# Kernel tuning notes

Hardware: AMD Instinct MI355X
Metric: run time of the kernel (lower is better)

The kernel has to match this reference:

```python
import jax, jax.numpy as jnp
import numpy as np

N = 4194304  # nodes
B = 16384    # graphs
D = 2        # spatial dim
EPS = 1e-12  # F.normalize eps


def _mlp(x, W1, b1, W2, b2, W3, b3, W4, b4, W5, b5):
    h = jax.nn.relu(x @ W1.T + b1)
    h = jax.nn.relu(h @ W2.T + b2)
    h = jax.nn.relu(h @ W3.T + b3)
    h = jax.nn.relu(h @ W4.T + b4)
    return h @ W5.T + b5  # [N,1]


def setup_inputs() -> dict:
    key = jax.random.key(0)
    ks = jax.random.split(key, 16)
    inp = {
        "t": jax.random.normal(ks[0], (N,), jnp.float32),
        "pos": jax.random.normal(ks[1], (N, D), jnp.float32),
        "poi_t": jax.random.normal(ks[2], (B,), jnp.float32),
        "poi_pos": jax.random.normal(ks[3], (B, D), jnp.float32),
        "batch": jnp.sort(jax.random.randint(ks[4], (N,), 0, B, jnp.int64)),
    }
    dims = [(10, 3), (20, 10), (10, 20), (5, 10), (1, 5)]
    for i, (o, ii) in enumerate(dims):
        s = 1.0 / np.sqrt(ii)
        inp[f"W{i+1}"] = jax.random.uniform(ks[5 + 2 * i], (o, ii), jnp.float32, -s, s)
        inp[f"b{i+1}"] = jax.random.uniform(ks[6 + 2 * i], (o,), jnp.float32, -s, s)
    return inp


def reference(t, pos, poi_t, poi_pos, batch, W1, b1, W2, b2, W3, b3, W4, b4, W5, b5):
    num_seg = poi_t.shape[0]
    diff_t = t - poi_t[batch]                      # [N]
    diff_pos = pos - poi_pos[batch]                # [N,D]
    r2 = jnp.sum(diff_pos ** 2, axis=1)            # [N]
    centroid = jax.ops.segment_sum(pos, batch, num_segments=num_seg)  # [B,D]
    diff_centroid = (centroid - poi_pos)[batch]    # [N,D]
    cosine = jnp.sum(diff_pos * diff_centroid, axis=1) / jnp.sqrt(
        r2 * jnp.sum(diff_centroid ** 2, axis=1))  # [N]
    feats = jnp.stack((diff_t, r2, cosine), axis=1)  # [N,3]
    weights = _mlp(feats, W1, b1, W2, b2, W3, b3, W4, b4, W5, b5)  # [N,1]
    norm = jnp.maximum(jnp.linalg.norm(diff_pos, axis=1, keepdims=True), EPS)
    unit = diff_pos / norm                         # F.normalize(diff_pos, dim=1)
    return jax.ops.segment_sum(weights * unit, batch, num_segments=num_seg)  # [B,D]
```

## Files before the change

kernel.cpp:

```cpp
#include <hip/hip_runtime.h>

#define NN 4194304
#define NB 16384

typedef _Float16 half4 __attribute__((ext_vector_type(4)));
typedef float floatx4 __attribute__((ext_vector_type(4)));
typedef unsigned int uint;

__device__ __forceinline__ uint pk_u32(float lo, float hi) {
  return __builtin_bit_cast(uint, __builtin_amdgcn_cvt_pkrtz(lo, hi));
}

__device__ __forceinline__ half4 relu_cvt(floatx4 d) {
  uint2 u;
  u.x = pk_u32(d[0], d[1]);
  u.y = pk_u32(d[2], d[3]);
  half4 h = __builtin_bit_cast(half4, u);
  return __builtin_elementwise_max(h, half4{0, 0, 0, 0});
}

template <int CTRL>
__device__ __forceinline__ float dpp_add(float x) {
  int y = __builtin_amdgcn_update_dpp(0, __builtin_bit_cast(int, x), CTRL,
                                      0xf, 0xf, true);
  return x + __builtin_bit_cast(float, y);
}
__device__ __forceinline__ float wave_sum(float x) {
  x = dpp_add<0x111>(x);
  x = dpp_add<0x112>(x);
  x = dpp_add<0x114>(x);
  x = dpp_add<0x118>(x);
  x = dpp_add<0x142>(x);
  x = dpp_add<0x143>(x);
  return x;
}

__device__ __forceinline__ void seg_atomic_add2(int b, float vx, float vy,
                                                float* __restrict__ out) {
  const int lane = threadIdx.x & 63;
  int b0 = __builtin_amdgcn_readfirstlane(b);
  if (__ballot(b == b0) == ~0ull) {
    float sx = wave_sum(vx);
    float sy = wave_sum(vy);
    if (lane == 63) {
      atomicAdd(&out[2 * b0], sx);
      atomicAdd(&out[2 * b0 + 1], sy);
    }
    return;
  }
  int bprev = __shfl_up(b, 1);
  bool head = (lane == 0) || (b != bprev);
  unsigned long long hb = __ballot(head);
  unsigned long long mask_le = hb << (63 - lane);
  int run_start = lane - __clzll(mask_le);
  float sx = vx, sy = vy;
#pragma unroll
  for (int off = 1; off < 64; off <<= 1) {
    float ox = __shfl_up(sx, off);
    float oy = __shfl_up(sy, off);
    if (lane - off >= run_start) { sx += ox; sy += oy; }
  }
  int bnext = __shfl_down(b, 1);
  bool tail = (lane == 63) || (b != bnext);
  if (tail) {
    atomicAdd(&out[2 * b], sx);
    atomicAdd(&out[2 * b + 1], sy);
  }
}

__global__ __launch_bounds__(256) void centroid_kernel(
    const float2* __restrict__ pos, const int* __restrict__ batch,
    float* __restrict__ csum) {
  int base = blockIdx.x * 1024 + threadIdx.x;
  int bi[4];
  float2 pv[4];
#pragma unroll
  for (int r = 0; r < 4; ++r) {
    bi[r] = batch[base + r * 256];
    pv[r] = pos[base + r * 256];
  }
#pragma unroll
  for (int r = 0; r < 4; ++r) seg_atomic_add2(bi[r], pv[r].x, pv[r].y, csum);
}

__global__ void prepack_kernel(
    const float* __restrict__ W1, const float* __restrict__ W2,
    const float* __restrict__ W3, const float* __restrict__ W4,
    const float* __restrict__ W5, const float* __restrict__ B1,
    const float* __restrict__ B2, const float* __restrict__ B3,
    const float* __restrict__ B4, const float* __restrict__ B5,
    uint2* __restrict__ Wf, float* __restrict__ csum,
    float* __restrict__ out) {
  if (blockIdx.x >= 3) {
    int z = (blockIdx.x - 3) * 256 + threadIdx.x;
    float4 zero{0.f, 0.f, 0.f, 0.f};
    if (z < 8192) ((float4*)csum)[z] = zero;
    else ((float4*)out)[z - 8192] = zero;
    return;
  }
  int p = blockIdx.x * 256 + threadIdx.x;
  if (p >= 448) return;
  int tile = p >> 6, lane = p & 63, row = lane & 15, kb = (lane >> 4) * 4;
  float v[4];
#pragma unroll
  for (int i = 0; i < 4; ++i) {
    int k = kb + i;
    float x = 0.f;
    switch (tile) {
      case 0:
        if (row < 10 && k < 3) x = W1[row * 3 + k];
        if (k == 3) { if (row < 10) x = B1[row]; else if (row == 10) x = 1.f; }
        break;
      case 1:
        if (k < 10) x = W2[row * 10 + k];
        else if (k == 10) x = B2[row];
        break;
      case 2:
        if (row < 4 && k < 10) x = W2[(16 + row) * 10 + k];
        if (k == 10) { if (row < 4) x = B2[16 + row]; else if (row == 4) x = 1.f; }
        break;
      case 3:
        if (row < 10 && k < 16) x = W3[row * 20 + k];
        break;
      case 4:
        if (row < 10 && k < 4) x = W3[row * 20 + 16 + k];
        if (k == 4) { if (row < 10) x = B3[row]; else if (row == 10) x = 1.f; }
        break;
      case 5:
        if (row < 5 && k < 10) x = W4[row * 10 + k];
        if (k == 10) { if (row < 5) x = B4[row]; else if (row == 5) x = 1.f; }
        break;
      default:
        if (row == 0 && k < 5) x = W5[k];
        if (row == 0 && k == 5) x = B5[0];
        break;
    }
    v[i] = x;
  }
  Wf[p] = uint2{pk_u32(v[0], v[1]), pk_u32(v[2], v[3])};
}

__device__ __forceinline__ floatx4 mfma16(half4 a, half4 b, floatx4 c) {
  return __builtin_amdgcn_mfma_f32_16x16x16f16(a, b, c, 0, 0, 0);
}

__global__ __launch_bounds__(256, 3) void main_kernel(
    const float* __restrict__ t, const float2* __restrict__ pos,
    const float* __restrict__ poi_t, const float2* __restrict__ poi_pos,
    const int* __restrict__ batch, const float2* __restrict__ csum2,
    const uint2* __restrict__ Wf, float* __restrict__ out) {
  const int tid = threadIdx.x;
  const int lane = tid & 63;
  const int col = lane & 15;
  const int koct = lane >> 4;

  int base = blockIdx.x * 1024 + tid;
  int bi[4];
  float tvv[4];
  float2 pv[4];
#pragma unroll
  for (int r = 0; r < 4; ++r) {
    bi[r] = batch[base + r * 256];
    tvv[r] = t[base + r * 256];
    pv[r] = pos[base + r * 256];
  }
  float2 ppr[4], csr[4];
  float ptg[4];
#pragma unroll
  for (int r = 0; r < 4; ++r) {
    ppr[r] = poi_pos[bi[r]];
    csr[r] = csum2[bi[r]];
    ptg[r] = poi_t[bi[r]];
  }

  half4 wa[7];
#pragma unroll
  for (int k = 0; k < 7; ++k)
    wa[k] = __builtin_bit_cast(half4, Wf[k * 64 + lane]);
  floatx4 cz{0.f, 0.f, 0.f, 0.f};

#pragma unroll
  for (int rp = 0; rp < 2; ++rp) {
    float dpx[2], dpy[2], f1v[2], invr[2];
    int fx[2], fy[2];
#pragma unroll
    for (int u = 0; u < 2; ++u) {
      int r = rp * 2 + u;
      float f0 = tvv[r] - ptg[r];
      float dcx = csr[r].x - ppr[r].x;
      float dcy = csr[r].y - ppr[r].y;
      float invc = rsqrtf(dcx * dcx + dcy * dcy);
      dpx[u] = pv[r].x - ppr[r].x;
      dpy[u] = pv[r].y - ppr[r].y;
      f1v[u] = dpx[u] * dpx[u] + dpy[u] * dpy[u];
      invr[u] = rsqrtf(f1v[u]);
      float f2 = (dpx[u] * dcx + dpy[u] * dcy) * invc * invr[u];
      fx[u] = (int)pk_u32(f0, f1v[u]);
      fy[u] = (int)pk_u32(f2, 1.0f);
    }

    half4 b1[8];
#pragma unroll
    for (int u = 0; u < 2; ++u)
#pragma unroll
      for (int g = 0; g < 4; ++g) {
        int src = g * 16 + col;
        uint2 fr;
        fr.x = (uint)__shfl(fx[u], src);
        fr.y = (uint)__shfl(fy[u], src);
        b1[u * 4 + g] = __builtin_bit_cast(half4, fr);
      }

    floatx4 d[8];
    half4 a[8];
#pragma unroll
    for (int c = 0; c < 8; ++c) d[c] = mfma16(wa[0], b1[c], cz);
#pragma unroll
    for (int c = 0; c < 8; ++c) a[c] = relu_cvt(d[c]);

    floatx4 d2[8];
    half4 a3a[8], a3b[8];
#pragma unroll
    for (int c = 0; c < 8; ++c) d2[c] = mfma16(wa[1], a[c], cz);
#pragma unroll
    for (int c = 0; c < 8; ++c) a3a[c] = relu_cvt(d2[c]);
#pragma unroll
    for (int c = 0; c < 8; ++c) d2[c] = mfma16(wa[2], a[c], cz);
#pragma unroll
    for (int c = 0; c < 8; ++c) a3b[c] = relu_cvt(d2[c]);

#pragma unroll
    for (int c = 0; c < 8; ++c) d[c] = mfma16(wa[3], a3a[c], cz);
#pragma unroll
    for (int c = 0; c < 8; ++c) d[c] = mfma16(wa[4], a3b[c], d[c]);
#pragma unroll
    for (int c = 0; c < 8; ++c) a[c] = relu_cvt(d[c]);

#pragma unroll
    for (int c = 0; c < 8; ++c) d[c] = mfma16(wa[5], a[c], cz);
#pragma unroll
    for (int c = 0; c < 8; ++c) a[c] = relu_cvt(d[c]);

#pragma unroll
    for (int c = 0; c < 8; ++c) d[c] = mfma16(wa[6], a[c], cz);

#pragma unroll
    for (int u = 0; u < 2; ++u) {
      float wg0 = __shfl(d[u * 4 + 0][0], col);
      float wg1 = __shfl(d[u * 4 + 1][0], col);
      float wg2 = __shfl(d[u * 4 + 2][0], col);
      float wg3 = __shfl(d[u * 4 + 3][0], col);
      float w = wg0;
      w = (koct == 1) ? wg1 : w;
      w = (koct == 2) ? wg2 : w;
      w = (koct == 3) ? wg3 : w;
      float invn = (f1v[u] > 0.f) ? invr[u] : 0.f;
      seg_atomic_add2(bi[rp * 2 + u], w * dpx[u] * invn, w * dpy[u] * invn,
                      out);
    }
  }
}

extern "C" void kernel_launch(void* const* d_in, const int* in_sizes, int n_in,
                              void* d_out, int out_size, void* d_ws,
                              size_t ws_size, hipStream_t stream) {
  const float* t = (const float*)d_in[0];
  const float2* pos = (const float2*)d_in[1];
  const float* poi_t = (const float*)d_in[2];
  const float2* poi_pos = (const float2*)d_in[3];
  const int* batch = (const int*)d_in[4];
  const float* W1 = (const float*)d_in[5];
  const float* B1 = (const float*)d_in[6];
  const float* W2 = (const float*)d_in[7];
  const float* B2 = (const float*)d_in[8];
  const float* W3 = (const float*)d_in[9];
  const float* B3 = (const float*)d_in[10];
  const float* W4 = (const float*)d_in[11];
  const float* B4 = (const float*)d_in[12];
  const float* W5 = (const float*)d_in[13];
  const float* B5 = (const float*)d_in[14];
  float* out = (float*)d_out;

  float* csum = (float*)d_ws;
  uint2* Wf = (uint2*)(csum + 2 * NB);

  prepack_kernel<<<67, 256, 0, stream>>>(W1, W2, W3, W4, W5, B1, B2, B3, B4,
                                         B5, Wf, csum, out);
  centroid_kernel<<<NN / 1024, 256, 0, stream>>>(pos, batch, csum);
  main_kernel<<<NN / 1024, 256, 0, stream>>>(t, pos, poi_t, poi_pos, batch,
                                             (const float2*)csum, Wf, out);
}
```

Before: 50.23 us.

## Use persistent grid with software-prefetched next tile in centroid and main kernels

Both the centroid and main kernels now launch a fixed grid of 768 blocks that loop over 4096 work units instead of one block per unit. Each iteration prefetches the next unit's batch, t and pos values, and the main kernel also prefetches the gathered poi and centroid values, before the current unit's MLP and atomics. The goal is to hide global-load latency behind compute and cut block-launch overhead. The cost is higher register pressure from the double-buffered state, which could lower occupancy under the launch bounds of 3.

```diff
diff --git a/kernel.cpp b/kernel.cpp
--- a/kernel.cpp
+++ b/kernel.cpp
@@ -2,6 +2,8 @@
 
 #define NN 4194304
 #define NB 16384
+#define GRIDP 768
+#define NUNITS 4096
 
 typedef _Float16 half4 __attribute__((ext_vector_type(4)));
 typedef float floatx4 __attribute__((ext_vector_type(4)));
@@ -71,16 +73,36 @@
 __global__ __launch_bounds__(256) void centroid_kernel(
     const float2* __restrict__ pos, const int* __restrict__ batch,
     float* __restrict__ csum) {
-  int base = blockIdx.x * 1024 + threadIdx.x;
-  int bi[4];
-  float2 pv[4];
+  const int tid = threadIdx.x;
+  int u = blockIdx.x;
+  int biA[4];
+  float2 pvA[4];
+  int base = u * 1024 + tid;
 #pragma unroll
   for (int r = 0; r < 4; ++r) {
-    bi[r] = batch[base + r * 256];
-    pv[r] = pos[base + r * 256];
-  }
-#pragma unroll
-  for (int r = 0; r < 4; ++r) seg_atomic_add2(bi[r], pv[r].x, pv[r].y, csum);
+    biA[r] = batch[base + r * 256];
+    pvA[r] = pos[base + r * 256];
+  }
+  for (; u < NUNITS; u += GRIDP) {
+    int un = u + GRIDP;
+    int biB[4];
+    float2 pvB[4];
+    if (un < NUNITS) {
+      int nb = un * 1024 + tid;
+#pragma unroll
+      for (int r = 0; r < 4; ++r) {
+        biB[r] = batch[nb + r * 256];
+        pvB[r] = pos[nb + r * 256];
+      }
+    }
+#pragma unroll
+    for (int r = 0; r < 4; ++r)
+      seg_atomic_add2(biA[r], pvA[r].x, pvA[r].y, csum);
+    if (un < NUNITS) {
+#pragma unroll
+      for (int r = 0; r < 4; ++r) { biA[r] = biB[r]; pvA[r] = pvB[r]; }
+    }
+  }
 }
 
 __global__ void prepack_kernel(
@@ -154,109 +176,158 @@
   const int col = lane & 15;
   const int koct = lane >> 4;
 
-  int base = blockIdx.x * 1024 + tid;
-  int bi[4];
-  float tvv[4];
-  float2 pv[4];
-#pragma unroll
-  for (int r = 0; r < 4; ++r) {
-    bi[r] = batch[base + r * 256];
-    tvv[r] = t[base + r * 256];
-    pv[r] = pos[base + r * 256];
-  }
-  float2 ppr[4], csr[4];
-  float ptg[4];
-#pragma unroll
-  for (int r = 0; r < 4; ++r) {
-    ppr[r] = poi_pos[bi[r]];
-    csr[r] = csum2[bi[r]];
-    ptg[r] = poi_t[bi[r]];
-  }
-
   half4 wa[7];
 #pragma unroll
   for (int k = 0; k < 7; ++k)
     wa[k] = __builtin_bit_cast(half4, Wf[k * 64 + lane]);
   floatx4 cz{0.f, 0.f, 0.f, 0.f};
 
-#pragma unroll
-  for (int rp = 0; rp < 2; ++rp) {
-    float dpx[2], dpy[2], f1v[2], invr[2];
-    int fx[2], fy[2];
-#pragma unroll
-    for (int u = 0; u < 2; ++u) {
-      int r = rp * 2 + u;
-      float f0 = tvv[r] - ptg[r];
-      float dcx = csr[r].x - ppr[r].x;
-      float dcy = csr[r].y - ppr[r].y;
+  int u = blockIdx.x;
+  int biA[4];
+  float tvA[4];
+  float2 pvA[4];
+  {
+    int base = u * 1024 + tid;
+#pragma unroll
+    for (int r = 0; r < 4; ++r) {
+      biA[r] = batch[base + r * 256];
+      tvA[r] = t[base + r * 256];
+      pvA[r] = pos[base + r * 256];
+    }
+  }
+  float2 ppA[4], csA[4];
+  float ptA[4];
+#pragma unroll
+  for (int r = 0; r < 4; ++r) {
+    ppA[r] = poi_pos[biA[r]];
+    csA[r] = csum2[biA[r]];
+    ptA[r] = poi_t[biA[r]];
+  }
+
+  for (; u < NUNITS; u += GRIDP) {
+    const int un = u + GRIDP;
+    const bool hn = (un < NUNITS);
+
+    int biB[4];
+    float tvB[4];
+    float2 pvB[4];
+    if (hn) {
+      int nb = un * 1024 + tid;
+#pragma unroll
+      for (int r = 0; r < 4; ++r) {
+        biB[r] = batch[nb + r * 256];
+        tvB[r] = t[nb + r * 256];
+        pvB[r] = pos[nb + r * 256];
+      }
+    }
+
+    float dpx[4], dpy[4], f1v[4], invr[4];
+    int fx[4], fy[4];
+#pragma unroll
+    for (int r = 0; r < 4; ++r) {
+      float f0 = tvA[r] - ptA[r];
+      float dcx = csA[r].x - ppA[r].x;
+      float dcy = csA[r].y - ppA[r].y;
       float invc = rsqrtf(dcx * dcx + dcy * dcy);
-      dpx[u] = pv[r].x - ppr[r].x;
-      dpy[u] = pv[r].y - ppr[r].y;
-      f1v[u] = dpx[u] * dpx[u] + dpy[u] * dpy[u];
-      invr[u] = rsqrtf(f1v[u]);
-      float f2 = (dpx[u] * dcx + dpy[u] * dcy) * invc * invr[u];
-      fx[u] = (int)pk_u32(f0, f1v[u]);
-      fy[u] = (int)pk_u32(f2, 1.0f);
-    }
-
-    half4 b1[8];
-#pragma unroll
-    for (int u = 0; u < 2; ++u)
-#pragma unroll
-      for (int g = 0; g < 4; ++g) {
-        int src = g * 16 + col;
-        uint2 fr;
-        fr.x = (uint)__shfl(fx[u], src);
-        fr.y = (uint)__shfl(fy[u], src);
-        b1[u * 4 + g] = __builtin_bit_cast(half4, fr);
-      }
-
-    floatx4 d[8];
-    half4 a[8];
-#pragma unroll
-    for (int c = 0; c < 8; ++c) d[c] = mfma16(wa[0], b1[c], cz);
-#pragma unroll
-    for (int c = 0; c < 8; ++c) a[c] = relu_cvt(d[c]);
-
-    floatx4 d2[8];
-    half4 a3a[8], a3b[8];
-#pragma unroll
-    for (int c = 0; c < 8; ++c) d2[c] = mfma16(wa[1], a[c], cz);
-#pragma unroll
-    for (int c = 0; c < 8; ++c) a3a[c] = relu_cvt(d2[c]);
-#pragma unroll
-    for (int c = 0; c < 8; ++c) d2[c] = mfma16(wa[2], a[c], cz);
-#pragma unroll
-    for (int c = 0; c < 8; ++c) a3b[c] = relu_cvt(d2[c]);
-
-#pragma unroll
-    for (int c = 0; c < 8; ++c) d[c] = mfma16(wa[3], a3a[c], cz);
-#pragma unroll
-    for (int c = 0; c < 8; ++c) d[c] = mfma16(wa[4], a3b[c], d[c]);
-#pragma unroll
-    for (int c = 0; c < 8; ++c) a[c] = relu_cvt(d[c]);
-
-#pragma unroll
-    for (int c = 0; c < 8; ++c) d[c] = mfma16(wa[5], a[c], cz);
-#pragma unroll
-    for (int c = 0; c < 8; ++c) a[c] = relu_cvt(d[c]);
-
-#pragma unroll
-    for (int c = 0; c < 8; ++c) d[c] = mfma16(wa[6], a[c], cz);
-
-#pragma unroll
-    for (int u = 0; u < 2; ++u) {
-      float wg0 = __shfl(d[u * 4 + 0][0], col);
-      float wg1 = __shfl(d[u * 4 + 1][0], col);
-      float wg2 = __shfl(d[u * 4 + 2][0], col);
-      float wg3 = __shfl(d[u * 4 + 3][0], col);
-      float w = wg0;
-      w = (koct == 1) ? wg1 : w;
-      w = (koct == 2) ? wg2 : w;
-      w = (koct == 3) ? wg3 : w;
-      float invn = (f1v[u] > 0.f) ? invr[u] : 0.f;
-      seg_atomic_add2(bi[rp * 2 + u], w * dpx[u] * invn, w * dpy[u] * invn,
+      dpx[r] = pvA[r].x - ppA[r].x;
+      dpy[r] = pvA[r].y - ppA[r].y;
+      f1v[r] = dpx[r] * dpx[r] + dpy[r] * dpy[r];
+      invr[r] = rsqrtf(f1v[r]);
+      float f2 = (dpx[r] * dcx + dpy[r] * dcy) * invc * invr[r];
+      fx[r] = (int)pk_u32(f0, f1v[r]);
+      fy[r] = (int)pk_u32(f2, 1.0f);
+    }
+
+    float wv[4];
+#pragma unroll
+    for (int rp = 0; rp < 2; ++rp) {
+      half4 b1[8];
+#pragma unroll
+      for (int uu = 0; uu < 2; ++uu)
+#pragma unroll
+        for (int g = 0; g < 4; ++g) {
+          int src = g * 16 + col;
+          uint2 fr;
+          fr.x = (uint)__shfl(fx[rp * 2 + uu], src);
+          fr.y = (uint)__shfl(fy[rp * 2 + uu], src);
+          b1[uu * 4 + g] = __builtin_bit_cast(half4, fr);
+        }
+
+      floatx4 d[8];
+      half4 a[8];
+#pragma unroll
+      for (int c = 0; c < 8; ++c) d[c] = mfma16(wa[0], b1[c], cz);
+#pragma unroll
+      for (int c = 0; c < 8; ++c) a[c] = relu_cvt(d[c]);
+
+      floatx4 d2[8];
+      half4 a3a[8], a3b[8];
+#pragma unroll
+      for (int c = 0; c < 8; ++c) d2[c] = mfma16(wa[1], a[c], cz);
+#pragma unroll
+      for (int c = 0; c < 8; ++c) a3a[c] = relu_cvt(d2[c]);
+#pragma unroll
+      for (int c = 0; c < 8; ++c) d2[c] = mfma16(wa[2], a[c], cz);
+#pragma unroll
+      for (int c = 0; c < 8; ++c) a3b[c] = relu_cvt(d2[c]);
+
+#pragma unroll
+      for (int c = 0; c < 8; ++c) d[c] = mfma16(wa[3], a3a[c], cz);
+#pragma unroll
+      for (int c = 0; c < 8; ++c) d[c] = mfma16(wa[4], a3b[c], d[c]);
+#pragma unroll
+      for (int c = 0; c < 8; ++c) a[c] = relu_cvt(d[c]);
+
+#pragma unroll
+      for (int c = 0; c < 8; ++c) d[c] = mfma16(wa[5], a[c], cz);
+#pragma unroll
+      for (int c = 0; c < 8; ++c) a[c] = relu_cvt(d[c]);
+
+#pragma unroll
+      for (int c = 0; c < 8; ++c) d[c] = mfma16(wa[6], a[c], cz);
+
+#pragma unroll
+      for (int uu = 0; uu < 2; ++uu) {
+        float wg0 = __shfl(d[uu * 4 + 0][0], col);
+        float wg1 = __shfl(d[uu * 4 + 1][0], col);
+        float wg2 = __shfl(d[uu * 4 + 2][0], col);
+        float wg3 = __shfl(d[uu * 4 + 3][0], col);
+        float w = wg0;
+        w = (koct == 1) ? wg1 : w;
+        w = (koct == 2) ? wg2 : w;
+        w = (koct == 3) ? wg3 : w;
+        wv[rp * 2 + uu] = w;
+      }
+    }
+
+    float2 ppB[4], csB[4];
+    float ptB[4];
+    if (hn) {
+#pragma unroll
+      for (int r = 0; r < 4; ++r) {
+        ppB[r] = poi_pos[biB[r]];
+        csB[r] = csum2[biB[r]];
+        ptB[r] = poi_t[biB[r]];
+      }
+    }
+
+#pragma unroll
+    for (int r = 0; r < 4; ++r) {
+      float invn = (f1v[r] > 0.f) ? invr[r] : 0.f;
+      seg_atomic_add2(biA[r], wv[r] * dpx[r] * invn, wv[r] * dpy[r] * invn,
                       out);
+    }
+
+    if (hn) {
+#pragma unroll
+      for (int r = 0; r < 4; ++r) {
+        biA[r] = biB[r];
+        tvA[r] = tvB[r];
+        pvA[r] = pvB[r];
+        ppA[r] = ppB[r];
+        csA[r] = csB[r];
+        ptA[r] = ptB[r];
+      }
     }
   }
 }
@@ -286,7 +357,7 @@
 
   prepack_kernel<<<67, 256, 0, stream>>>(W1, W2, W3, W4, W5, B1, B2, B3, B4,
                                          B5, Wf, csum, out);
-  centroid_kernel<<<NN / 1024, 256, 0, stream>>>(pos, batch, csum);
-  main_kernel<<<NN / 1024, 256, 0, stream>>>(t, pos, poi_t, poi_pos, batch,
-                                             (const float2*)csum, Wf, out);
-}
+  centroid_kernel<<<GRIDP, 256, 0, stream>>>(pos, batch, csum);
+  main_kernel<<<GRIDP, 256, 0, stream>>>(t, pos, poi_t, poi_pos, batch,
+                                         (const float2*)csum, Wf, out);
+}
```

Measured after the change: 61.90 us. 1.23x slower.

## Fuse centroid and main kernels using a persistent grid barrier

Applied to the files above, without the earlier changes.

Merges the centroid segment-sum kernel and the MLP kernel into one persistent kernel of 1024 blocks, each handling 4096 nodes. Blocks first atomically accumulate centroids, then synchronise through a global atomic counter barrier before running the MLP. Batch and pos values stay in registers, so they are not re-read and one launch is saved. The barrier relies on all 1024 blocks being co-resident (256 CUs at 4 blocks each), and the larger per-thread register arrays add register pressure.

```diff
diff --git a/kernel.cpp b/kernel.cpp
--- a/kernel.cpp
+++ b/kernel.cpp
@@ -2,6 +2,7 @@
 
 #define NN 4194304
 #define NB 16384
+#define GRIDP 1024
 
 typedef _Float16 half4 __attribute__((ext_vector_type(4)));
 typedef float floatx4 __attribute__((ext_vector_type(4)));
@@ -68,21 +69,6 @@
   }
 }
 
-__global__ __launch_bounds__(256) void centroid_kernel(
-    const float2* __restrict__ pos, const int* __restrict__ batch,
-    float* __restrict__ csum) {
-  int base = blockIdx.x * 1024 + threadIdx.x;
-  int bi[4];
-  float2 pv[4];
-#pragma unroll
-  for (int r = 0; r < 4; ++r) {
-    bi[r] = batch[base + r * 256];
-    pv[r] = pos[base + r * 256];
-  }
-#pragma unroll
-  for (int r = 0; r < 4; ++r) seg_atomic_add2(bi[r], pv[r].x, pv[r].y, csum);
-}
-
 __global__ void prepack_kernel(
     const float* __restrict__ W1, const float* __restrict__ W2,
     const float* __restrict__ W3, const float* __restrict__ W4,
@@ -90,7 +76,7 @@
     const float* __restrict__ B2, const float* __restrict__ B3,
     const float* __restrict__ B4, const float* __restrict__ B5,
     uint2* __restrict__ Wf, float* __restrict__ csum,
-    float* __restrict__ out) {
+    float* __restrict__ out, uint* __restrict__ bar) {
   if (blockIdx.x >= 3) {
     int z = (blockIdx.x - 3) * 256 + threadIdx.x;
     float4 zero{0.f, 0.f, 0.f, 0.f};
@@ -99,7 +85,8 @@
     return;
   }
   int p = blockIdx.x * 256 + threadIdx.x;
-  if (p >= 448) return;
+  if (p >= 456) return;
+  if (p >= 448) { bar[p - 448] = 0u; return; }
   int tile = p >> 6, lane = p & 63, row = lane & 15, kb = (lane >> 4) * 4;
   float v[4];
 #pragma unroll
@@ -144,34 +131,45 @@
   return __builtin_amdgcn_mfma_f32_16x16x16f16(a, b, c, 0, 0, 0);
 }
 
-__global__ __launch_bounds__(256, 3) void main_kernel(
+__global__ __launch_bounds__(256, 4) void fused_kernel(
     const float* __restrict__ t, const float2* __restrict__ pos,
     const float* __restrict__ poi_t, const float2* __restrict__ poi_pos,
-    const int* __restrict__ batch, const float2* __restrict__ csum2,
-    const uint2* __restrict__ Wf, float* __restrict__ out) {
+    const int* __restrict__ batch, const uint2* __restrict__ Wf,
+    float* __restrict__ csum, float* __restrict__ out,
+    uint* __restrict__ bar) {
   const int tid = threadIdx.x;
   const int lane = tid & 63;
   const int col = lane & 15;
   const int koct = lane >> 4;
-
-  int base = blockIdx.x * 1024 + tid;
-  int bi[4];
-  float tvv[4];
-  float2 pv[4];
-#pragma unroll
-  for (int r = 0; r < 4; ++r) {
+  const float2* csum2 = (const float2*)csum;
+
+  int base = blockIdx.x * 4096 + tid;
+  int bi[16];
+  float2 pv[16];
+#pragma unroll
+  for (int r = 0; r < 16; ++r) {
     bi[r] = batch[base + r * 256];
-    tvv[r] = t[base + r * 256];
     pv[r] = pos[base + r * 256];
   }
-  float2 ppr[4], csr[4];
-  float ptg[4];
-#pragma unroll
-  for (int r = 0; r < 4; ++r) {
-    ppr[r] = poi_pos[bi[r]];
-    csr[r] = csum2[bi[r]];
-    ptg[r] = poi_t[bi[r]];
-  }
+
+#pragma unroll
+  for (int r = 0; r < 16; ++r)
+    seg_atomic_add2(bi[r], pv[r].x, pv[r].y, csum);
+
+  __syncthreads();
+  if (tid == 0) {
+    uint prev = __hip_atomic_fetch_add(&bar[0], 1u, __ATOMIC_ACQ_REL,
+                                       __HIP_MEMORY_SCOPE_AGENT);
+    if (prev == GRIDP - 1) {
+      __hip_atomic_store(&bar[1], 1u, __ATOMIC_RELEASE,
+                         __HIP_MEMORY_SCOPE_AGENT);
+    } else {
+      while (__hip_atomic_load(&bar[1], __ATOMIC_ACQUIRE,
+                               __HIP_MEMORY_SCOPE_AGENT) == 0u)
+        __builtin_amdgcn_s_sleep(2);
+    }
+  }
+  __syncthreads();
 
   half4 wa[7];
 #pragma unroll
@@ -180,18 +178,22 @@
   floatx4 cz{0.f, 0.f, 0.f, 0.f};
 
 #pragma unroll
-  for (int rp = 0; rp < 2; ++rp) {
+  for (int rp = 0; rp < 8; ++rp) {
     float dpx[2], dpy[2], f1v[2], invr[2];
     int fx[2], fy[2];
 #pragma unroll
     for (int u = 0; u < 2; ++u) {
       int r = rp * 2 + u;
-      float f0 = tvv[r] - ptg[r];
-      float dcx = csr[r].x - ppr[r].x;
-      float dcy = csr[r].y - ppr[r].y;
+      float tv = t[base + r * 256];
+      float2 pp = poi_pos[bi[r]];
+      float2 cs = csum2[bi[r]];
+      float pt = poi_t[bi[r]];
+      float f0 = tv - pt;
+      float dcx = cs.x - pp.x;
+      float dcy = cs.y - pp.y;
       float invc = rsqrtf(dcx * dcx + dcy * dcy);
-      dpx[u] = pv[r].x - ppr[r].x;
-      dpy[u] = pv[r].y - ppr[r].y;
+      dpx[u] = pv[r].x - pp.x;
+      dpy[u] = pv[r].y - pp.y;
       f1v[u] = dpx[u] * dpx[u] + dpy[u] * dpy[u];
       invr[u] = rsqrtf(f1v[u]);
       float f2 = (dpx[u] * dcx + dpy[u] * dcy) * invc * invr[u];
@@ -283,10 +285,10 @@
 
   float* csum = (float*)d_ws;
   uint2* Wf = (uint2*)(csum + 2 * NB);
+  uint* bar = (uint*)(Wf + 448);
 
   prepack_kernel<<<67, 256, 0, stream>>>(W1, W2, W3, W4, W5, B1, B2, B3, B4,
-                                         B5, Wf, csum, out);
-  centroid_kernel<<<NN / 1024, 256, 0, stream>>>(pos, batch, csum);
-  main_kernel<<<NN / 1024, 256, 0, stream>>>(t, pos, poi_t, poi_pos, batch,
-                                             (const float2*)csum, Wf, out);
-}
+                                         B5, Wf, csum, out, bar);
+  fused_kernel<<<GRIDP, 256, 0, stream>>>(t, pos, poi_t, poi_pos, batch, Wf,
+                                          csum, out, bar);
+}
```

Measured after the change: 179.1 us. 3.56x slower.
